# Optimization experiments

Hardware: AMD Instinct MI355X
Metric: run time of the kernel (lower is better)

## Reference

```python
import jax, jax.numpy as jnp
import numpy as np

NEG_SLOPE_ATT = 0.2   # GATConv internal leaky_relu slope
NEG_SLOPE_ACT = 0.01  # f.leaky_relu default
LN_EPS = 1e-5

N_NODES, N_EDGES, F_IN = 50000, 400000, 256
HEADS, C1, C2, N_CLS = 4, 256, 128, 32


def gat_conv(x, src, dst, W, a_src, a_dst, bias, concat):
    """PyG GATConv (self-loops already appended to src/dst)."""
    N = x.shape[0]
    H, C = a_src.shape
    h = (x @ W.T).reshape(N, H, C)                      # [N,H,C]
    s = (h * a_src[None]).sum(-1)                       # [N,H] alpha_src
    d = (h * a_dst[None]).sum(-1)                       # [N,H] alpha_dst
    e = jax.nn.leaky_relu(s[src] + d[dst], NEG_SLOPE_ATT)  # [E,H]
    emax = jax.ops.segment_max(e, dst, num_segments=N)
    emax = jnp.where(jnp.isfinite(emax), emax, 0.0)
    p = jnp.exp(e - emax[dst])
    denom = jax.ops.segment_sum(p, dst, num_segments=N)
    alpha = p / (denom[dst] + 1e-16)                    # segment softmax over dst
    out = jax.ops.segment_sum(alpha[:, :, None] * h[src], dst, num_segments=N)
    out = out.reshape(N, H * C) if concat else out.mean(axis=1)
    return out + bias


def layer_norm(x, g, b):
    mu = x.mean(-1, keepdims=True)
    var = jnp.var(x, axis=-1, keepdims=True)
    return (x - mu) / jnp.sqrt(var + LN_EPS) * g + b


def setup_inputs() -> dict:
    key = jax.random.key(0)
    ks = jax.random.split(key, 24)
    def g(k, shape, scale=0.1):
        return jax.random.normal(k, shape, dtype=jnp.float32) * scale
    inp = {
        "x": g(ks[0], (N_NODES, F_IN), 1.0),
        "edge_src": jax.random.randint(ks[1], (N_EDGES,), 0, N_NODES, dtype=jnp.int32),
        "edge_dst": jax.random.randint(ks[2], (N_EDGES,), 0, N_NODES, dtype=jnp.int32),
        # layer 1: in F_IN -> H*C1 (concat)
        "W1": g(ks[3], (HEADS * C1, F_IN)),
        "a_src1": g(ks[4], (HEADS, C1)), "a_dst1": g(ks[5], (HEADS, C1)),
        "b1": jnp.zeros((HEADS * C1,), jnp.float32),
        "ln1_g": jnp.ones((HEADS * C1,), jnp.float32), "ln1_b": jnp.zeros((HEADS * C1,), jnp.float32),
        # layer 2: in H*C1 -> H*C2 (concat)
        "W2": g(ks[6], (HEADS * C2, HEADS * C1)),
        "a_src2": g(ks[7], (HEADS, C2)), "a_dst2": g(ks[8], (HEADS, C2)),
        "b2": jnp.zeros((HEADS * C2,), jnp.float32),
        "ln2_g": jnp.ones((HEADS * C2,), jnp.float32), "ln2_b": jnp.zeros((HEADS * C2,), jnp.float32),
        # layer 3: in H*C2 -> N_CLS (heads=1, mean/no-concat)
        "W3": g(ks[9], (1 * N_CLS, HEADS * C2)),
        "a_src3": g(ks[10], (1, N_CLS)), "a_dst3": g(ks[11], (1, N_CLS)),
        "b3": jnp.zeros((N_CLS,), jnp.float32),
        "ln3_g": jnp.ones((N_CLS,), jnp.float32), "ln3_b": jnp.zeros((N_CLS,), jnp.float32),
    }
    return inp


def reference(x, edge_src, edge_dst,
              W1, a_src1, a_dst1, b1, ln1_g, ln1_b,
              W2, a_src2, a_dst2, b2, ln2_g, ln2_b,
              W3, a_src3, a_dst3, b3, ln3_g, ln3_b):
    N = x.shape[0]
    loops = jnp.arange(N, dtype=edge_src.dtype)  # GATConv add_self_loops=True
    src = jnp.concatenate([edge_src, loops])
    dst = jnp.concatenate([edge_dst, loops])
    # dropout layers are identity in eval mode
    h = gat_conv(x, src, dst, W1, a_src1, a_dst1, b1, True)
    h = jax.nn.leaky_relu(layer_norm(h, ln1_g, ln1_b), NEG_SLOPE_ACT)
    h = gat_conv(h, src, dst, W2, a_src2, a_dst2, b2, True)
    h = jax.nn.leaky_relu(layer_norm(h, ln2_g, ln2_b), NEG_SLOPE_ACT)
    h = gat_conv(h, src, dst, W3, a_src3, a_dst3, b3, False)
    h = layer_norm(h, ln3_g, ln3_b)
    return jax.nn.log_softmax(h, axis=1)
```

## Files before the change

### kernel.cpp

```cpp
#include <hip/hip_runtime.h>
#include <math.h>


#define NEG_ATT 0.2f
#define NEG_ACT 0.01f

typedef __attribute__((ext_vector_type(8))) short bf16x8;
typedef __attribute__((ext_vector_type(8))) unsigned short u16x8;
typedef __attribute__((ext_vector_type(4))) float f32x4;

__device__ __forceinline__ float bf2f(unsigned short u) {
  union { unsigned int i; float f; } c; c.i = ((unsigned int)u) << 16; return c.f;
}
__device__ __forceinline__ unsigned short f2bf(float f) {
  union { float f; unsigned int i; } c; c.f = f;
  unsigned int r = c.i + 0x7FFFu + ((c.i >> 16) & 1u);
  return (unsigned short)(r >> 16);
}

__global__ void cvt_kernel(const float* __restrict__ in,
                           unsigned short* __restrict__ out, int n8) {
  int i = blockIdx.x * 256 + threadIdx.x;
  if (i >= n8) return;
  float4 v0 = reinterpret_cast<const float4*>(in)[i * 2];
  float4 v1 = reinterpret_cast<const float4*>(in)[i * 2 + 1];
  ushort4 o0 = make_ushort4(f2bf(v0.x), f2bf(v0.y), f2bf(v0.z), f2bf(v0.w));
  ushort4 o1 = make_ushort4(f2bf(v1.x), f2bf(v1.y), f2bf(v1.z), f2bf(v1.w));
  reinterpret_cast<ushort4*>(out)[i * 2] = o0;
  reinterpret_cast<ushort4*>(out)[i * 2 + 1] = o1;
}

__global__ __launch_bounds__(256) void qb_kernel(const float* __restrict__ W1,
    const float* __restrict__ as1, const float* __restrict__ ad1,
    unsigned short* __restrict__ Qb) {
  int r = blockIdx.x;
  int k = threadIdx.x;
  if (r >= 8) { Qb[r * 256 + k] = 0; return; }
  int h = r & 3;
  const float* av = (r >> 2) ? ad1 : as1;
  float acc = 0.f;
#pragma unroll 8
  for (int c = 0; c < 256; c++)
    acc += W1[((size_t)(h * 256 + c)) * 256 + k] * av[h * 256 + c];
  Qb[r * 256 + k] = f2bf(acc);
}

__global__ void hist_kernel(const int* __restrict__ edge_dst,
                            int* __restrict__ cnt, int E, int N) {
  int e = blockIdx.x * 256 + threadIdx.x;
  if (e >= E + N) return;
  int dn = (e < E) ? edge_dst[e] : (e - E);
  atomicAdd(&cnt[dn], 1);
}

__global__ __launch_bounds__(256) void scan1_kernel(
    const int* __restrict__ cnt, int* __restrict__ bsum, int N) {
  __shared__ int sd_[256];
  int i = blockIdx.x * 256 + threadIdx.x;
  int v = (i < N) ? cnt[i] : 0;
  sd_[threadIdx.x] = v;
  __syncthreads();
#pragma unroll
  for (int off = 128; off; off >>= 1) {
    if (threadIdx.x < off) sd_[threadIdx.x] += sd_[threadIdx.x + off];
    __syncthreads();
  }
  if (threadIdx.x == 0) bsum[blockIdx.x] = sd_[0];
}

__global__ __launch_bounds__(256) void scan2_kernel(
    const int* __restrict__ bsum, int* __restrict__ boff,
    int* __restrict__ row_ptr, int NB, int N) {
  __shared__ int sd_[256];
  int t = threadIdx.x;
  int v = (t < NB) ? bsum[t] : 0;
  sd_[t] = v;
  __syncthreads();
#pragma unroll
  for (int off = 1; off < 256; off <<= 1) {
    int u = (t >= off) ? sd_[t - off] : 0;
    __syncthreads();
    sd_[t] += u;
    __syncthreads();
  }
  if (t < NB) boff[t] = sd_[t] - v;
  if (t == 255) row_ptr[N] = sd_[255];
}

__global__ __launch_bounds__(256) void scan3_kernel(
    const int* __restrict__ cnt, const int* __restrict__ boff,
    int* __restrict__ row_ptr, int* __restrict__ cur, int N) {
  __shared__ int sd_[256];
  int t = threadIdx.x;
  int i = blockIdx.x * 256 + t;
  int v = (i < N) ? cnt[i] : 0;
  sd_[t] = v;
  __syncthreads();
#pragma unroll
  for (int off = 1; off < 256; off <<= 1) {
    int u = (t >= off) ? sd_[t - off] : 0;
    __syncthreads();
    sd_[t] += u;
    __syncthreads();
  }
  if (i < N) {
    int val = boff[blockIdx.x] + sd_[t] - v;
    row_ptr[i] = val;
    cur[i] = val;
  }
}

__global__ void scatter_kernel(const int* __restrict__ edge_src,
                               const int* __restrict__ edge_dst,
                               int* __restrict__ cur,
                               int* __restrict__ src_sorted, int E, int N) {
  int e = blockIdx.x * 256 + threadIdx.x;
  if (e >= E + N) return;
  int sn, dn;
  if (e < E) { sn = edge_src[e]; dn = edge_dst[e]; }
  else       { sn = dn = e - E; }
  int pos = atomicAdd(&cur[dn], 1);
  src_sorted[pos] = sn;
}

#define GLOBAL_AS __attribute__((address_space(1)))
#define LDS_AS __attribute__((address_space(3)))

__device__ __forceinline__ void gload_lds16(const void* g, void* l) {
  __builtin_amdgcn_global_load_lds((const GLOBAL_AS unsigned int*)g,
                                   (LDS_AS unsigned int*)l, 16, 0, 0);
}

template <int BM, int BN, int WM, int WN, bool F32OUT>
__global__ __launch_bounds__(256) void gemm_mfma(
    const unsigned short* __restrict__ A, const unsigned short* __restrict__ B,
    void* __restrict__ Cv, const float* __restrict__ bias,
    int M, int N, int K, int lda, int ldb, int ldc,
    long long aZ, long long bZ, long long cZ, int biasZ) {
  constexpr int BK = 64;
  constexpr int FM = BM / (WM * 16);
  constexpr int FN = BN / (WN * 16);
  const int flat = blockIdx.x + gridDim.x * (blockIdx.y + gridDim.y * blockIdx.z);
  const int nwg = gridDim.x * gridDim.y * gridDim.z;
  const int xcd = flat & 7, slot = flat >> 3;
  const int q = nwg >> 3, r = nwg & 7;
  const int wgid = (xcd < r ? xcd * (q + 1) : r * (q + 1) + (xcd - r) * q) + slot;
  const int nx = gridDim.x;
  const int per_z = nx * gridDim.y;
  const int bz = wgid / per_z;
  const int rem = wgid - bz * per_z;
  const int bmi = rem / nx;
  const int bni = rem - bmi * nx;

  A += (size_t)bz * aZ;
  B += (size_t)bz * bZ;
  const size_t cbase = (size_t)bz * cZ;
  __shared__ unsigned short As[BM * BK];
  __shared__ unsigned short Bs[BN * BK];
  const int tid = threadIdx.x;
  const int w = tid >> 6, lane = tid & 63;
  const int wm = w / WN, wn = w % WN;
  const int bm = bmi * BM;
  const int bn = bni * BN;
  const int l15 = lane & 15, l4 = lane >> 4;

  f32x4 acc[FM][FN] = {};

  constexpr int CHA = BM * BK / 8;
  constexpr int CHB = BN * BK / 8;

  for (int k0 = 0; k0 < K; k0 += BK) {
#pragma unroll
    for (int c0 = 0; c0 < CHA; c0 += 256) {
      int c = c0 + tid;
      if (CHA - c0 >= 256 || tid < CHA - c0) {
        int cl = c ^ ((c >> 3) & 7);
        int row = cl >> 3;
        int kk = (cl & 7) * 8;
        int gr = bm + row; if (gr > M - 1) gr = M - 1;
        gload_lds16(A + (size_t)gr * lda + k0 + kk,
                    As + (size_t)(c0 + (tid & ~63)) * 8);
      }
    }
#pragma unroll
    for (int c0 = 0; c0 < CHB; c0 += 256) {
      int c = c0 + tid;
      if (CHB - c0 >= 256 || tid < CHB - c0) {
        int cl = c ^ ((c >> 3) & 7);
        int row = cl >> 3;
        int kk = (cl & 7) * 8;
        gload_lds16(B + (size_t)(bn + row) * ldb + k0 + kk,
                    Bs + (size_t)(c0 + (tid & ~63)) * 8);
      }
    }
    __syncthreads();
#pragma unroll
    for (int ks = 0; ks < 2; ks++) {
      bf16x8 af[FM], bfr[FN];
#pragma unroll
      for (int i = 0; i < FM; i++) {
        int row = wm * (FM * 16) + i * 16 + l15;
        int byte = row * (BK * 2) + ks * 64 + l4 * 16;
        byte ^= ((byte >> 7) & 7) << 4;
        af[i] = *reinterpret_cast<const bf16x8*>((const char*)As + byte);
      }
#pragma unroll
      for (int i = 0; i < FN; i++) {
        int row = wn * (FN * 16) + i * 16 + l15;
        int byte = row * (BK * 2) + ks * 64 + l4 * 16;
        byte ^= ((byte >> 7) & 7) << 4;
        bfr[i] = *reinterpret_cast<const bf16x8*>((const char*)Bs + byte);
      }
#pragma unroll
      for (int i = 0; i < FM; i++)
#pragma unroll
        for (int jn = 0; jn < FN; jn++)
          acc[i][jn] = __builtin_amdgcn_mfma_f32_16x16x32_bf16(
              af[i], bfr[jn], acc[i][jn], 0, 0, 0);
    }
    __syncthreads();
  }
#pragma unroll
  for (int i = 0; i < FM; i++) {
#pragma unroll
    for (int jn = 0; jn < FN; jn++) {
      int col = bn + wn * (FN * 16) + jn * 16 + l15;
      float bv = bias ? bias[biasZ * bz + col] : 0.f;
#pragma unroll
      for (int r2 = 0; r2 < 4; r2++) {
        int m = bm + wm * (FM * 16) + i * 16 + l4 * 4 + r2;
        if (m < M) {
          float val = acc[i][jn][r2] + bv;
          if constexpr (F32OUT)
            ((float*)Cv)[cbase + (size_t)m * ldc + col] = val;
          else
            ((unsigned short*)Cv)[cbase + (size_t)m * ldc + col] = f2bf(val);
        }
      }
    }
  }
}

__global__ __launch_bounds__(256) void aggx_kernel(
    const int* __restrict__ row_ptr, const int* __restrict__ src_sorted,
    const float* __restrict__ sd1, const unsigned short* __restrict__ xb,
    unsigned short* __restrict__ y, int N) {
  __shared__ float alds[4][2][64][4];
  int w = threadIdx.x >> 6, lane = threadIdx.x & 63;
  int n = blockIdx.x * 4 + w;
  if (n >= N) return;
  int beg = row_ptr[n], end = row_ptr[n + 1];
  float4 dv = *reinterpret_cast<const float4*>(sd1 + (size_t)n * 16 + 4);

  auto compE = [&](int t, float e[4]) {
    if (t < end) {
      int sj = src_sorted[t];
      float4 sv = *reinterpret_cast<const float4*>(sd1 + (size_t)sj * 16);
      e[0] = sv.x + dv.x; e[1] = sv.y + dv.y;
      e[2] = sv.z + dv.z; e[3] = sv.w + dv.w;
#pragma unroll
      for (int h = 0; h < 4; h++) e[h] = e[h] > 0.f ? e[h] : NEG_ATT * e[h];
    } else {
      e[0] = e[1] = e[2] = e[3] = -1e30f;
    }
  };

  float mx[4] = {-1e30f, -1e30f, -1e30f, -1e30f};
  for (int cb = beg; cb < end; cb += 64) {
    float e[4]; compE(cb + lane, e);
#pragma unroll
    for (int h = 0; h < 4; h++) {
      float m = e[h];
#pragma unroll
      for (int o = 32; o; o >>= 1) m = fmaxf(m, __shfl_xor(m, o));
      mx[h] = fmaxf(mx[h], m);
    }
  }
  float den[4] = {0.f, 0.f, 0.f, 0.f};
  for (int cb = beg; cb < end; cb += 64) {
    float e[4]; compE(cb + lane, e);
#pragma unroll
    for (int h = 0; h < 4; h++) {
      float p = __expf(e[h] - mx[h]);
#pragma unroll
      for (int o = 32; o; o >>= 1) p += __shfl_xor(p, o);
      den[h] += p;
    }
  }
  float ia[4];
#pragma unroll
  for (int h = 0; h < 4; h++) ia[h] = 1.0f / (den[h] + 1e-16f);

  float acc[4][4] = {};
  for (int cb = beg; cb < end; cb += 64) {
    float e[4]; compE(cb + lane, e);
    int pb = ((cb - beg) >> 6) & 1;
    float4 al;
    al.x = __expf(e[0] - mx[0]) * ia[0];
    al.y = __expf(e[1] - mx[1]) * ia[1];
    al.z = __expf(e[2] - mx[2]) * ia[2];
    al.w = __expf(e[3] - mx[3]) * ia[3];
    *reinterpret_cast<float4*>(alds[w][pb][lane]) = al;
    int cd = end - cb; if (cd > 64) cd = 64;
    for (int j = 0; j < cd; j++) {
      float4 a4 = *reinterpret_cast<const float4*>(alds[w][pb][j]);
      int sj = src_sorted[cb + j];
      ushort4 xv = *reinterpret_cast<const ushort4*>(
          xb + (size_t)sj * 256 + lane * 4);
      float x0 = bf2f(xv.x), x1 = bf2f(xv.y), x2 = bf2f(xv.z), x3 = bf2f(xv.w);
      float ar[4] = {a4.x, a4.y, a4.z, a4.w};
#pragma unroll
      for (int h = 0; h < 4; h++) {
        acc[h][0] = fmaf(ar[h], x0, acc[h][0]);
        acc[h][1] = fmaf(ar[h], x1, acc[h][1]);
        acc[h][2] = fmaf(ar[h], x2, acc[h][2]);
        acc[h][3] = fmaf(ar[h], x3, acc[h][3]);
      }
    }
  }
#pragma unroll
  for (int h = 0; h < 4; h++) {
    ushort4 o = make_ushort4(f2bf(acc[h][0]), f2bf(acc[h][1]),
                             f2bf(acc[h][2]), f2bf(acc[h][3]));
    *reinterpret_cast<ushort4*>(y + (size_t)n * 1024 + h * 256 + lane * 4) = o;
  }
}

__global__ __launch_bounds__(256) void agg2m_kernel(
    const int* __restrict__ row_ptr, const int* __restrict__ src_sorted,
    const float* __restrict__ s2, const float* __restrict__ d2,
    const unsigned short* __restrict__ h2, const float* __restrict__ bias,
    const float* __restrict__ ln_g, const float* __restrict__ ln_b,
    unsigned short* __restrict__ outb, int N) {
  __shared__ float alds[4][2][64][4];
  int w = threadIdx.x >> 6, lane = threadIdx.x & 63;
  int n = blockIdx.x * 4 + w;
  if (n >= N) return;
  int beg = row_ptr[n], end = row_ptr[n + 1];
  int head = lane >> 4, c0 = lane * 8;
  float4 dv = *reinterpret_cast<const float4*>(d2 + (size_t)n * 4);

  auto compE = [&](int t, float e[4]) {
    if (t < end) {
      int sj = src_sorted[t];
      float4 sv = *reinterpret_cast<const float4*>(s2 + (size_t)sj * 4);
      e[0] = sv.x + dv.x; e[1] = sv.y + dv.y;
      e[2] = sv.z + dv.z; e[3] = sv.w + dv.w;
#pragma unroll
      for (int h = 0; h < 4; h++) e[h] = e[h] > 0.f ? e[h] : NEG_ATT * e[h];
    } else {
      e[0] = e[1] = e[2] = e[3] = -1e30f;
    }
  };

  float mx[4] = {-1e30f, -1e30f, -1e30f, -1e30f};
  for (int cb = beg; cb < end; cb += 64) {
    float e[4]; compE(cb + lane, e);
#pragma unroll
    for (int h = 0; h < 4; h++) {
      float m = e[h];
#pragma unroll
      for (int o = 32; o; o >>= 1) m = fmaxf(m, __shfl_xor(m, o));
      mx[h] = fmaxf(mx[h], m);
    }
  }
  float den[4] = {0.f, 0.f, 0.f, 0.f};
  for (int cb = beg; cb < end; cb += 64) {
    float e[4]; compE(cb + lane, e);
#pragma unroll
    for (int h = 0; h < 4; h++) {
      float p = __expf(e[h] - mx[h]);
#pragma unroll
      for (int o = 32; o; o >>= 1) p += __shfl_xor(p, o);
      den[h] += p;
    }
  }
  float ia[4];
#pragma unroll
  for (int h = 0; h < 4; h++) ia[h] = 1.0f / (den[h] + 1e-16f);

  float acc[8] = {};
  for (int cb = beg; cb < end; cb += 64) {
    float e[4]; compE(cb + lane, e);
    int pb = ((cb - beg) >> 6) & 1;
    float4 al;
    al.x = __expf(e[0] - mx[0]) * ia[0];
    al.y = __expf(e[1] - mx[1]) * ia[1];
    al.z = __expf(e[2] - mx[2]) * ia[2];
    al.w = __expf(e[3] - mx[3]) * ia[3];
    *reinterpret_cast<float4*>(alds[w][pb][lane]) = al;
    int cd = end - cb; if (cd > 64) cd = 64;
    for (int j = 0; j < cd; j++) {
      float a = alds[w][pb][j][head];
      int sj = src_sorted[cb + j];
      u16x8 xv = *reinterpret_cast<const u16x8*>(h2 + (size_t)sj * 512 + c0);
#pragma unroll
      for (int i = 0; i < 8; i++)
        acc[i] = fmaf(a, bf2f(xv[i]), acc[i]);
    }
  }
  float v[8], s1 = 0.f, sq = 0.f;
#pragma unroll
  for (int i = 0; i < 8; i++) {
    v[i] = acc[i] + bias[c0 + i];
    s1 += v[i]; sq += v[i] * v[i];
  }
#pragma unroll
  for (int o = 32; o; o >>= 1) { s1 += __shfl_xor(s1, o); sq += __shfl_xor(sq, o); }
  float mean = s1 * (1.0f / 512.0f);
  float var = sq * (1.0f / 512.0f) - mean * mean;
  float rstd = rsqrtf(var + 1e-5f);
  u16x8 ov;
#pragma unroll
  for (int i = 0; i < 8; i++) {
    float yv = (v[i] - mean) * rstd * ln_g[c0 + i] + ln_b[c0 + i];
    yv = yv > 0.f ? yv : NEG_ACT * yv;
    ov[i] = f2bf(yv);
  }
  *reinterpret_cast<u16x8*>(outb + (size_t)n * 512 + c0) = ov;
}

__global__ __launch_bounds__(256) void ln1024_kernel(
    const unsigned short* __restrict__ z, const float* __restrict__ ln_g,
    const float* __restrict__ ln_b, unsigned short* __restrict__ outb, int N) {
  int n = blockIdx.x;
  int tid = threadIdx.x;
  int c0 = tid * 4;
  ushort4 zv = *reinterpret_cast<const ushort4*>(z + (size_t)n * 1024 + c0);
  float v[4] = {bf2f(zv.x), bf2f(zv.y), bf2f(zv.z), bf2f(zv.w)};
  float s1 = v[0] + v[1] + v[2] + v[3];
  float sq = v[0]*v[0] + v[1]*v[1] + v[2]*v[2] + v[3]*v[3];
#pragma unroll
  for (int o = 32; o; o >>= 1) { s1 += __shfl_down(s1, o); sq += __shfl_down(sq, o); }
  __shared__ float r1[4], r2[4];
  int wave = tid >> 6, lane = tid & 63;
  if (lane == 0) { r1[wave] = s1; r2[wave] = sq; }
  __syncthreads();
  float t1 = r1[0] + r1[1] + r1[2] + r1[3];
  float t2 = r2[0] + r2[1] + r2[2] + r2[3];
  float mean = t1 * (1.0f / 1024.0f);
  float var = t2 * (1.0f / 1024.0f) - mean * mean;
  float rstd = rsqrtf(var + 1e-5f);
  ushort4 ov;
  float y0 = (v[0] - mean) * rstd * ln_g[c0 + 0] + ln_b[c0 + 0];
  float y1 = (v[1] - mean) * rstd * ln_g[c0 + 1] + ln_b[c0 + 1];
  float y2 = (v[2] - mean) * rstd * ln_g[c0 + 2] + ln_b[c0 + 2];
  float y3 = (v[3] - mean) * rstd * ln_g[c0 + 3] + ln_b[c0 + 3];
  ov.x = f2bf(y0 > 0.f ? y0 : NEG_ACT * y0);
  ov.y = f2bf(y1 > 0.f ? y1 : NEG_ACT * y1);
  ov.z = f2bf(y2 > 0.f ? y2 : NEG_ACT * y2);
  ov.w = f2bf(y3 > 0.f ? y3 : NEG_ACT * y3);
  *reinterpret_cast<ushort4*>(outb + (size_t)n * 1024 + c0) = ov;
}

__global__ __launch_bounds__(256) void sd128_kernel(
    const unsigned short* __restrict__ h, const float* __restrict__ a_src,
    const float* __restrict__ a_dst, float* __restrict__ s,
    float* __restrict__ d, int N) {
  int n = blockIdx.x;
  int head = threadIdx.x >> 6;
  int lane = threadIdx.x & 63;
  const unsigned short* row = h + (size_t)n * 512 + head * 128 + lane * 2;
  ushort2 u = *reinterpret_cast<const ushort2*>(row);
  float2 a = *reinterpret_cast<const float2*>(a_src + head * 128 + lane * 2);
  float2 b = *reinterpret_cast<const float2*>(a_dst + head * 128 + lane * 2);
  float ss = bf2f(u.x) * a.x + bf2f(u.y) * a.y;
  float dd = bf2f(u.x) * b.x + bf2f(u.y) * b.y;
#pragma unroll
  for (int o = 32; o; o >>= 1) { ss += __shfl_down(ss, o); dd += __shfl_down(dd, o); }
  if (lane == 0) { s[(size_t)n * 4 + head] = ss; d[(size_t)n * 4 + head] = dd; }
}

__global__ __launch_bounds__(256) void sd32_kernel(
    const unsigned short* __restrict__ h, const float* __restrict__ a_src,
    const float* __restrict__ a_dst, float* __restrict__ s,
    float* __restrict__ d, int N) {
  int idx = blockIdx.x * 256 + threadIdx.x;
  int n = idx >> 5, c = idx & 31;
  if (n >= N) return;
  float v = bf2f(h[(size_t)n * 32 + c]);
  float ss = v * a_src[c], dd = v * a_dst[c];
#pragma unroll
  for (int o = 16; o; o >>= 1) { ss += __shfl_xor(ss, o, 32); dd += __shfl_xor(dd, o, 32); }
  if (c == 0) { s[n] = ss; d[n] = dd; }
}

__global__ void stats_kernel(const int* __restrict__ row_ptr,
    const int* __restrict__ src_sorted, const float* __restrict__ s,
    const float* __restrict__ d, float* __restrict__ p_sorted,
    float* __restrict__ inv_den, int N) {
  int idx = blockIdx.x * blockDim.x + threadIdx.x;
  if (idx >= N) return;
  int n = idx;
  int beg = row_ptr[n], end = row_ptr[n + 1];
  float dn = d[n];
  float mx = -1e30f;
  for (int j = beg; j < end; j++) {
    float v = s[src_sorted[j]] + dn;
    v = v > 0.f ? v : NEG_ATT * v;
    mx = fmaxf(mx, v);
  }
  float den = 0.f;
  for (int j = beg; j < end; j++) {
    float v = s[src_sorted[j]] + dn;
    v = v > 0.f ? v : NEG_ATT * v;
    float p = __expf(v - mx);
    p_sorted[j] = p;
    den += p;
  }
  inv_den[n] = 1.0f / (den + 1e-16f);
}

__global__ __launch_bounds__(256) void final_kernel(
    const int* __restrict__ row_ptr, const int* __restrict__ src_sorted,
    const float* __restrict__ p_sorted, const float* __restrict__ inv_den,
    const unsigned short* __restrict__ h3, const float* __restrict__ b3,
    const float* __restrict__ g3, const float* __restrict__ bb3,
    float* __restrict__ out, int N) {
  int idx = blockIdx.x * 256 + threadIdx.x;
  int n = idx >> 5, c = idx & 31;
  if (n >= N) return;
  int beg = row_ptr[n], end = row_ptr[n + 1];
  float acc = 0.f;
  for (int j = beg; j < end; j++)
    acc = fmaf(p_sorted[j], bf2f(h3[(size_t)src_sorted[j] * 32 + c]), acc);
  float v = acc * inv_den[n] + b3[c];
  float s1 = v, s2 = v * v;
#pragma unroll
  for (int o = 16; o; o >>= 1) { s1 += __shfl_xor(s1, o, 32); s2 += __shfl_xor(s2, o, 32); }
  float mean = s1 * (1.f / 32.f), var = s2 * (1.f / 32.f) - mean * mean;
  float y = (v - mean) * rsqrtf(var + 1e-5f) * g3[c] + bb3[c];
  float mx = y;
#pragma unroll
  for (int o = 16; o; o >>= 1) mx = fmaxf(mx, __shfl_xor(mx, o, 32));
  float ex = __expf(y - mx), se = ex;
#pragma unroll
  for (int o = 16; o; o >>= 1) se += __shfl_xor(se, o, 32);
  out[(size_t)n * 32 + c] = y - mx - __logf(se);
}

extern "C" void kernel_launch(void* const* d_in, const int* in_sizes, int n_in,
                              void* d_out, int out_size, void* d_ws,
                              size_t ws_size, hipStream_t stream) {
  const float* x   = (const float*)d_in[0];
  const int* esrc  = (const int*)d_in[1];
  const int* edst  = (const int*)d_in[2];
  const float* W1  = (const float*)d_in[3];
  const float* as1 = (const float*)d_in[4];
  const float* ad1 = (const float*)d_in[5];
  const float* b1  = (const float*)d_in[6];
  const float* g1  = (const float*)d_in[7];
  const float* bb1 = (const float*)d_in[8];
  const float* W2  = (const float*)d_in[9];
  const float* as2 = (const float*)d_in[10];
  const float* ad2 = (const float*)d_in[11];
  const float* b2  = (const float*)d_in[12];
  const float* g2  = (const float*)d_in[13];
  const float* bb2 = (const float*)d_in[14];
  const float* W3  = (const float*)d_in[15];
  const float* as3 = (const float*)d_in[16];
  const float* ad3 = (const float*)d_in[17];
  const float* b3  = (const float*)d_in[18];
  const float* g3  = (const float*)d_in[19];
  const float* bb3 = (const float*)d_in[20];
  float* out = (float*)d_out;

  const int Nn = in_sizes[0] / 256;
  const int E  = in_sizes[1];
  const int Etot = E + Nn;
  const int NB = (Nn + 255) / 256;

  char* ws = (char*)d_ws;
  size_t off = 0;
  auto alloc = [&](size_t bytes) -> char* {
    char* p = ws + off;
    off += (bytes + 255) & ~(size_t)255;
    return p;
  };
  int* cnt        = (int*)alloc((size_t)(Nn + 1) * 4);
  int* cur        = (int*)alloc((size_t)(Nn + 1) * 4);
  int* row_ptr    = (int*)alloc((size_t)(Nn + 1) * 4);
  int* bsum       = (int*)alloc(256 * 4);
  int* boff       = (int*)alloc(256 * 4);
  int* src_sorted = (int*)alloc((size_t)Etot * 4);
  float* sd1   = (float*)alloc((size_t)Nn * 16 * 4);
  float* s2    = (float*)alloc((size_t)Nn * 4 * 4);
  float* d2    = (float*)alloc((size_t)Nn * 4 * 4);
  float* s3    = (float*)alloc((size_t)Nn * 4);
  float* d3    = (float*)alloc((size_t)Nn * 4);
  float* invd3 = (float*)alloc((size_t)Nn * 4);
  float* p3    = (float*)alloc((size_t)Etot * 4);
  unsigned short* W1b = (unsigned short*)alloc((size_t)1024 * 256 * 2);
  unsigned short* W2b = (unsigned short*)alloc((size_t)512 * 1024 * 2);
  unsigned short* W3b = (unsigned short*)alloc((size_t)32 * 512 * 2);
  unsigned short* Qb  = (unsigned short*)alloc((size_t)16 * 256 * 2);
  unsigned short* h3  = (unsigned short*)alloc((size_t)Nn * 32 * 2);
  unsigned short* regA = (unsigned short*)alloc((size_t)Nn * 1024 * 2);
  unsigned short* regB = (unsigned short*)alloc((size_t)Nn * 1024 * 2);
  unsigned short* y    = regA;
  unsigned short* act1 = regA;
  unsigned short* act2 = regA;
  unsigned short* xb   = regB;
  unsigned short* z1   = regB;
  unsigned short* h2   = regB;

  const int mb = (Nn + 127) / 128;

  cvt_kernel<<<(Nn * 256 / 8 + 255) / 256, 256, 0, stream>>>(x, xb, Nn * 256 / 8);
  cvt_kernel<<<(1024 * 256 / 8 + 255) / 256, 256, 0, stream>>>(W1, W1b, 1024 * 256 / 8);
  cvt_kernel<<<(512 * 1024 / 8 + 255) / 256, 256, 0, stream>>>(W2, W2b, 512 * 1024 / 8);
  cvt_kernel<<<(32 * 512 / 8 + 255) / 256, 256, 0, stream>>>(W3, W3b, 32 * 512 / 8);
  qb_kernel<<<16, 256, 0, stream>>>(W1, as1, ad1, Qb);

  hipMemsetAsync(cnt, 0, (size_t)(Nn + 1) * 4, stream);
  int eb = (Etot + 255) / 256;
  hist_kernel<<<eb, 256, 0, stream>>>(edst, cnt, E, Nn);
  scan1_kernel<<<NB, 256, 0, stream>>>(cnt, bsum, Nn);
  scan2_kernel<<<1, 256, 0, stream>>>(bsum, boff, row_ptr, NB, Nn);
  scan3_kernel<<<NB, 256, 0, stream>>>(cnt, boff, row_ptr, cur, Nn);
  scatter_kernel<<<eb, 256, 0, stream>>>(esrc, edst, cur, src_sorted, E, Nn);

  gemm_mfma<128, 16, 4, 1, true><<<dim3(1, mb, 1), 256, 0, stream>>>(
      xb, Qb, sd1, nullptr, Nn, 16, 256, 256, 256, 16, 0, 0, 0, 0);
  aggx_kernel<<<(Nn + 3) / 4, 256, 0, stream>>>(row_ptr, src_sorted, sd1, xb, y, Nn);
  gemm_mfma<128, 128, 2, 2, false><<<dim3(2, mb, 4), 256, 0, stream>>>(
      y, W1b, z1, b1, Nn, 256, 256, 1024, 256, 1024, 256LL, 256LL * 256, 256LL, 256);
  ln1024_kernel<<<Nn, 256, 0, stream>>>(z1, g1, bb1, act1, Nn);

  gemm_mfma<128, 128, 2, 2, false><<<dim3(4, mb, 1), 256, 0, stream>>>(
      act1, W2b, h2, nullptr, Nn, 512, 1024, 1024, 1024, 512, 0, 0, 0, 0);
  sd128_kernel<<<Nn, 256, 0, stream>>>(h2, as2, ad2, s2, d2, Nn);
  agg2m_kernel<<<(Nn + 3) / 4, 256, 0, stream>>>(row_ptr, src_sorted, s2, d2,
                                                 h2, b2, g2, bb2, act2, Nn);

  gemm_mfma<128, 32, 4, 1, false><<<dim3(1, mb, 1), 256, 0, stream>>>(
      act2, W3b, h3, nullptr, Nn, 32, 512, 512, 512, 32, 0, 0, 0, 0);
  sd32_kernel<<<(Nn * 32 + 255) / 256, 256, 0, stream>>>(h3, as3, ad3, s3, d3, Nn);
  stats_kernel<<<(Nn + 255) / 256, 256, 0, stream>>>(row_ptr, src_sorted,
                                                     s3, d3, p3, invd3, Nn);
  final_kernel<<<(Nn * 32 + 255) / 256, 256, 0, stream>>>(row_ptr, src_sorted,
      p3, invd3, h3, b3, g3, bb3, out, Nn);
}
```

Baseline: 682.8 us.

## Double-buffer GEMM LDS, fuse attention dot products into GEMM epilogue, merge conversions

Merges the four fp32-to-bf16 conversion launches into one kernel. Adds LDS double buffering to the MFMA GEMM so the next K tile is loaded while the current one is computed. Replaces the separate sd128 and sd32 kernels with an epilogue in the layer-2 and layer-3 GEMMs that computes the per-head attention dot products from fp32 accumulators, reduces them with shuffles and accumulates them with atomics into a buffer zeroed by a new memset. The double buffer doubles LDS use per block, which may lower occupancy, and the atomics add contention and make the summation order nondeterministic.

Measured after the change: 709.4 us. +3.9%, slower.

```diff
diff --git a/kernel.cpp b/kernel.cpp
--- a/kernel.cpp
+++ b/kernel.cpp
@@ -18,16 +18,23 @@
   return (unsigned short)(r >> 16);
 }
 
-__global__ void cvt_kernel(const float* __restrict__ in,
-                           unsigned short* __restrict__ out, int n8) {
+__global__ void cvt4_kernel(const float* __restrict__ i0, unsigned short* o0, int n0,
+                            const float* __restrict__ i1, unsigned short* o1, int n1,
+                            const float* __restrict__ i2, unsigned short* o2, int n2,
+                            const float* __restrict__ i3, unsigned short* o3, int n3) {
   int i = blockIdx.x * 256 + threadIdx.x;
-  if (i >= n8) return;
-  float4 v0 = reinterpret_cast<const float4*>(in)[i * 2];
-  float4 v1 = reinterpret_cast<const float4*>(in)[i * 2 + 1];
-  ushort4 o0 = make_ushort4(f2bf(v0.x), f2bf(v0.y), f2bf(v0.z), f2bf(v0.w));
-  ushort4 o1 = make_ushort4(f2bf(v1.x), f2bf(v1.y), f2bf(v1.z), f2bf(v1.w));
-  reinterpret_cast<ushort4*>(out)[i * 2] = o0;
-  reinterpret_cast<ushort4*>(out)[i * 2 + 1] = o1;
+  const float* in; unsigned short* out; int idx;
+  if (i < n0) { in = i0; out = o0; idx = i; }
+  else if (i < n0 + n1) { in = i1; out = o1; idx = i - n0; }
+  else if (i < n0 + n1 + n2) { in = i2; out = o2; idx = i - n0 - n1; }
+  else if (i < n0 + n1 + n2 + n3) { in = i3; out = o3; idx = i - n0 - n1 - n2; }
+  else return;
+  float4 v0 = reinterpret_cast<const float4*>(in)[idx * 2];
+  float4 v1 = reinterpret_cast<const float4*>(in)[idx * 2 + 1];
+  ushort4 q0 = make_ushort4(f2bf(v0.x), f2bf(v0.y), f2bf(v0.z), f2bf(v0.w));
+  ushort4 q1 = make_ushort4(f2bf(v1.x), f2bf(v1.y), f2bf(v1.z), f2bf(v1.w));
+  reinterpret_cast<ushort4*>(out)[idx * 2] = q0;
+  reinterpret_cast<ushort4*>(out)[idx * 2 + 1] = q1;
 }
 
 __global__ __launch_bounds__(256) void qb_kernel(const float* __restrict__ W1,
@@ -131,12 +138,14 @@
                                    (LDS_AS unsigned int*)l, 16, 0, 0);
 }
 
-template <int BM, int BN, int WM, int WN, bool F32OUT>
+template <int BM, int BN, int WM, int WN, bool F32OUT, bool SDMODE>
 __global__ __launch_bounds__(256) void gemm_mfma(
     const unsigned short* __restrict__ A, const unsigned short* __restrict__ B,
     void* __restrict__ Cv, const float* __restrict__ bias,
     int M, int N, int K, int lda, int ldb, int ldc,
-    long long aZ, long long bZ, long long cZ, int biasZ) {
+    long long aZ, long long bZ, long long cZ, int biasZ,
+    float* __restrict__ sOut, float* __restrict__ dOut,
+    const float* __restrict__ a_s, const float* __restrict__ a_d, int H) {
   constexpr int BK = 64;
   constexpr int FM = BM / (WM * 16);
   constexpr int FN = BN / (WN * 16);
@@ -155,8 +164,8 @@
   A += (size_t)bz * aZ;
   B += (size_t)bz * bZ;
   const size_t cbase = (size_t)bz * cZ;
-  __shared__ unsigned short As[BM * BK];
-  __shared__ unsigned short Bs[BN * BK];
+  __shared__ unsigned short As[2][BM * BK];
+  __shared__ unsigned short Bs[2][BN * BK];
   const int tid = threadIdx.x;
   const int w = tid >> 6, lane = tid & 63;
   const int wm = w / WN, wn = w % WN;
@@ -169,7 +178,7 @@
   constexpr int CHA = BM * BK / 8;
   constexpr int CHB = BN * BK / 8;
 
-  for (int k0 = 0; k0 < K; k0 += BK) {
+  auto STAGE = [&](int buf, int k0) {
 #pragma unroll
     for (int c0 = 0; c0 < CHA; c0 += 256) {
       int c = c0 + tid;
@@ -179,7 +188,7 @@
         int kk = (cl & 7) * 8;
         int gr = bm + row; if (gr > M - 1) gr = M - 1;
         gload_lds16(A + (size_t)gr * lda + k0 + kk,
-                    As + (size_t)(c0 + (tid & ~63)) * 8);
+                    As[buf] + (size_t)(c0 + (tid & ~63)) * 8);
       }
     }
 #pragma unroll
@@ -190,10 +199,16 @@
         int row = cl >> 3;
         int kk = (cl & 7) * 8;
         gload_lds16(B + (size_t)(bn + row) * ldb + k0 + kk,
-                    Bs + (size_t)(c0 + (tid & ~63)) * 8);
+                    Bs[buf] + (size_t)(c0 + (tid & ~63)) * 8);
       }
     }
-    __syncthreads();
+  };
+
+  STAGE(0, 0);
+  __syncthreads();
+  int cur = 0;
+  for (int k0 = 0; k0 < K; k0 += BK) {
+    if (k0 + BK < K) STAGE(cur ^ 1, k0 + BK);
 #pragma unroll
     for (int ks = 0; ks < 2; ks++) {
       bf16x8 af[FM], bfr[FN];
@@ -202,14 +217,14 @@
         int row = wm * (FM * 16) + i * 16 + l15;
         int byte = row * (BK * 2) + ks * 64 + l4 * 16;
         byte ^= ((byte >> 7) & 7) << 4;
-        af[i] = *reinterpret_cast<const bf16x8*>((const char*)As + byte);
+        af[i] = *reinterpret_cast<const bf16x8*>((const char*)As[cur] + byte);
       }
 #pragma unroll
       for (int i = 0; i < FN; i++) {
         int row = wn * (FN * 16) + i * 16 + l15;
         int byte = row * (BK * 2) + ks * 64 + l4 * 16;
         byte ^= ((byte >> 7) & 7) << 4;
-        bfr[i] = *reinterpret_cast<const bf16x8*>((const char*)Bs + byte);
+        bfr[i] = *reinterpret_cast<const bf16x8*>((const char*)Bs[cur] + byte);
       }
 #pragma unroll
       for (int i = 0; i < FM; i++)
@@ -219,6 +234,40 @@
               af[i], bfr[jn], acc[i][jn], 0, 0, 0);
     }
     __syncthreads();
+    cur ^= 1;
+  }
+  if constexpr (SDMODE) {
+    float aws[FN], awd[FN];
+#pragma unroll
+    for (int jn = 0; jn < FN; jn++) {
+      int c = wn * (FN * 16) + jn * 16 + l15;
+      aws[jn] = a_s[bni * BN + c];
+      awd[jn] = a_d[bni * BN + c];
+    }
+#pragma unroll
+    for (int i = 0; i < FM; i++) {
+#pragma unroll
+      for (int r2 = 0; r2 < 4; r2++) {
+        float ps = 0.f, pd = 0.f;
+#pragma unroll
+        for (int jn = 0; jn < FN; jn++) {
+          ps = fmaf(acc[i][jn][r2], aws[jn], ps);
+          pd = fmaf(acc[i][jn][r2], awd[jn], pd);
+        }
+#pragma unroll
+        for (int o = 1; o < 16; o <<= 1) {
+          ps += __shfl_xor(ps, o);
+          pd += __shfl_xor(pd, o);
+        }
+        if (l15 == 0) {
+          int m = bm + wm * (FM * 16) + i * 16 + l4 * 4 + r2;
+          if (m < M) {
+            atomicAdd(&sOut[(size_t)m * H + bni], ps);
+            atomicAdd(&dOut[(size_t)m * H + bni], pd);
+          }
+        }
+      }
+    }
   }
 #pragma unroll
   for (int i = 0; i < FM; i++) {
@@ -451,38 +500,6 @@
   ov.z = f2bf(y2 > 0.f ? y2 : NEG_ACT * y2);
   ov.w = f2bf(y3 > 0.f ? y3 : NEG_ACT * y3);
   *reinterpret_cast<ushort4*>(outb + (size_t)n * 1024 + c0) = ov;
-}
-
-__global__ __launch_bounds__(256) void sd128_kernel(
-    const unsigned short* __restrict__ h, const float* __restrict__ a_src,
-    const float* __restrict__ a_dst, float* __restrict__ s,
-    float* __restrict__ d, int N) {
-  int n = blockIdx.x;
-  int head = threadIdx.x >> 6;
-  int lane = threadIdx.x & 63;
-  const unsigned short* row = h + (size_t)n * 512 + head * 128 + lane * 2;
-  ushort2 u = *reinterpret_cast<const ushort2*>(row);
-  float2 a = *reinterpret_cast<const float2*>(a_src + head * 128 + lane * 2);
-  float2 b = *reinterpret_cast<const float2*>(a_dst + head * 128 + lane * 2);
-  float ss = bf2f(u.x) * a.x + bf2f(u.y) * a.y;
-  float dd = bf2f(u.x) * b.x + bf2f(u.y) * b.y;
-#pragma unroll
-  for (int o = 32; o; o >>= 1) { ss += __shfl_down(ss, o); dd += __shfl_down(dd, o); }
-  if (lane == 0) { s[(size_t)n * 4 + head] = ss; d[(size_t)n * 4 + head] = dd; }
-}
-
-__global__ __launch_bounds__(256) void sd32_kernel(
-    const unsigned short* __restrict__ h, const float* __restrict__ a_src,
-    const float* __restrict__ a_dst, float* __restrict__ s,
-    float* __restrict__ d, int N) {
-  int idx = blockIdx.x * 256 + threadIdx.x;
-  int n = idx >> 5, c = idx & 31;
-  if (n >= N) return;
-  float v = bf2f(h[(size_t)n * 32 + c]);
-  float ss = v * a_src[c], dd = v * a_dst[c];
-#pragma unroll
-  for (int o = 16; o; o >>= 1) { ss += __shfl_xor(ss, o, 32); dd += __shfl_xor(dd, o, 32); }
-  if (c == 0) { s[n] = ss; d[n] = dd; }
 }
 
 __global__ void stats_kernel(const int* __restrict__ row_ptr,
@@ -584,10 +601,11 @@
   int* boff       = (int*)alloc(256 * 4);
   int* src_sorted = (int*)alloc((size_t)Etot * 4);
   float* sd1   = (float*)alloc((size_t)Nn * 16 * 4);
-  float* s2    = (float*)alloc((size_t)Nn * 4 * 4);
-  float* d2    = (float*)alloc((size_t)Nn * 4 * 4);
-  float* s3    = (float*)alloc((size_t)Nn * 4);
-  float* d3    = (float*)alloc((size_t)Nn * 4);
+  float* sdbuf = (float*)alloc((size_t)Nn * 10 * 4);
+  float* s2 = sdbuf;
+  float* d2 = sdbuf + (size_t)Nn * 4;
+  float* s3 = sdbuf + (size_t)Nn * 8;
+  float* d3 = sdbuf + (size_t)Nn * 9;
   float* invd3 = (float*)alloc((size_t)Nn * 4);
   float* p3    = (float*)alloc((size_t)Etot * 4);
   unsigned short* W1b = (unsigned short*)alloc((size_t)1024 * 256 * 2);
@@ -606,13 +624,16 @@
 
   const int mb = (Nn + 127) / 128;
 
-  cvt_kernel<<<(Nn * 256 / 8 + 255) / 256, 256, 0, stream>>>(x, xb, Nn * 256 / 8);
-  cvt_kernel<<<(1024 * 256 / 8 + 255) / 256, 256, 0, stream>>>(W1, W1b, 1024 * 256 / 8);
-  cvt_kernel<<<(512 * 1024 / 8 + 255) / 256, 256, 0, stream>>>(W2, W2b, 512 * 1024 / 8);
-  cvt_kernel<<<(32 * 512 / 8 + 255) / 256, 256, 0, stream>>>(W3, W3b, 32 * 512 / 8);
+  {
+    int n0 = Nn * 256 / 8, n1 = 1024 * 256 / 8, n2 = 512 * 1024 / 8, n3 = 32 * 512 / 8;
+    int tot = n0 + n1 + n2 + n3;
+    cvt4_kernel<<<(tot + 255) / 256, 256, 0, stream>>>(
+        x, xb, n0, W1, W1b, n1, W2, W2b, n2, W3, W3b, n3);
+  }
   qb_kernel<<<16, 256, 0, stream>>>(W1, as1, ad1, Qb);
 
   hipMemsetAsync(cnt, 0, (size_t)(Nn + 1) * 4, stream);
+  hipMemsetAsync(sdbuf, 0, (size_t)Nn * 10 * 4, stream);
   int eb = (Etot + 255) / 256;
   hist_kernel<<<eb, 256, 0, stream>>>(edst, cnt, E, Nn);
   scan1_kernel<<<NB, 256, 0, stream>>>(cnt, bsum, Nn);
@@ -620,22 +641,24 @@
   scan3_kernel<<<NB, 256, 0, stream>>>(cnt, boff, row_ptr, cur, Nn);
   scatter_kernel<<<eb, 256, 0, stream>>>(esrc, edst, cur, src_sorted, E, Nn);
 
-  gemm_mfma<128, 16, 4, 1, true><<<dim3(1, mb, 1), 256, 0, stream>>>(
-      xb, Qb, sd1, nullptr, Nn, 16, 256, 256, 256, 16, 0, 0, 0, 0);
+  gemm_mfma<128, 16, 4, 1, true, false><<<dim3(1, mb, 1), 256, 0, stream>>>(
+      xb, Qb, sd1, nullptr, Nn, 16, 256, 256, 256, 16, 0, 0, 0, 0,
+      nullptr, nullptr, nullptr, nullptr, 0);
   aggx_kernel<<<(Nn + 3) / 4, 256, 0, stream>>>(row_ptr, src_sorted, sd1, xb, y, Nn);
-  gemm_mfma<128, 128, 2, 2, false><<<dim3(2, mb, 4), 256, 0, stream>>>(
-      y, W1b, z1, b1, Nn, 256, 256, 1024, 256, 1024, 256LL, 256LL * 256, 256LL, 256);
+  gemm_mfma<128, 128, 2, 2, false, false><<<dim3(2, mb, 4), 256, 0, stream>>>(
+      y, W1b, z1, b1, Nn, 256, 256, 1024, 256, 1024, 256LL, 256LL * 256, 256LL, 256,
+      nullptr, nullptr, nullptr, nullptr, 0);
   ln1024_kernel<<<Nn, 256, 0, stream>>>(z1, g1, bb1, act1, Nn);
 
-  gemm_mfma<128, 128, 2, 2, false><<<dim3(4, mb, 1), 256, 0, stream>>>(
-      act1, W2b, h2, nullptr, Nn, 512, 1024, 1024, 1024, 512, 0, 0, 0, 0);
-  sd128_kernel<<<Nn, 256, 0, stream>>>(h2, as2, ad2, s2, d2, Nn);
+  gemm_mfma<128, 128, 2, 2, false, true><<<dim3(4, mb, 1), 256, 0, stream>>>(
+      act1, W2b, h2, nullptr, Nn, 512, 1024, 1024, 1024, 512, 0, 0, 0, 0,
+      s2, d2, as2, ad2, 4);
   agg2m_kernel<<<(Nn + 3) / 4, 256, 0, stream>>>(row_ptr, src_sorted, s2, d2,
                                                  h2, b2, g2, bb2, act2, Nn);
 
-  gemm_mfma<128, 32, 4, 1, false><<<dim3(1, mb, 1), 256, 0, stream>>>(
-      act2, W3b, h3, nullptr, Nn, 32, 512, 512, 512, 32, 0, 0, 0, 0);
-  sd32_kernel<<<(Nn * 32 + 255) / 256, 256, 0, stream>>>(h3, as3, ad3, s3, d3, Nn);
+  gemm_mfma<128, 32, 4, 1, false, true><<<dim3(1, mb, 1), 256, 0, stream>>>(
+      act2, W3b, h3, nullptr, Nn, 32, 512, 512, 512, 32, 0, 0, 0, 0,
+      s3, d3, as3, ad3, 1);
   stats_kernel<<<(Nn + 255) / 256, 256, 0, stream>>>(row_ptr, src_sorted,
                                                      s3, d3, p3, invd3, Nn);
   final_kernel<<<(Nn * 32 + 255) / 256, 256, 0, stream>>>(row_ptr, src_sorted,
```
